# Performance work log

Hardware: AMD Instinct MI355X
Metric: run time of the kernel (lower is better)

Reference implementation:

```python
import jax, jax.numpy as jnp
import numpy as np

N = 50000   # nodes
E = 400000  # directed edges (line-graph nodes)
LE = 1600000  # line-graph edges
B = 256     # graphs in batch
F = 64      # n_feats
ED = 16     # edge_dim
NIT = 3     # n_iter
SF = 6 * F  # LinearBlock hidden


def _seg_softmax(vals, seg, num):
    # numerically stable segment softmax (PyG softmax)
    m = jax.ops.segment_max(vals, seg, num_segments=num)
    e = jnp.exp(vals - m[seg])
    s = jax.ops.segment_sum(e, seg, num_segments=num)
    return e / (s[seg] + 1e-16)


def _gat_pool(out, lg_src, lg_dst, batch, gat_W, att_src, att_dst, gat_bias):
    # PyG GATConv(F, 1): heads=1, add_self_loops=True, negative_slope=0.2
    xw = out @ gat_W                       # [E, 1]
    sl = jnp.arange(E, dtype=lg_src.dtype)
    src = jnp.concatenate([lg_src, sl])
    dst = jnp.concatenate([lg_dst, sl])
    a_s = xw[:, 0] * att_src[0]
    a_d = xw[:, 0] * att_dst[0]
    alpha = jax.nn.leaky_relu(a_s[src] + a_d[dst], negative_slope=0.2)
    coef = _seg_softmax(alpha, dst, E)     # softmax over incoming line-edges
    xc = jax.ops.segment_sum(coef[:, None] * xw[src], dst, num_segments=E) + gat_bias  # [E,1]
    # GlobalAttentionPool: segment softmax over batch, then weighted sum pool
    sc = _seg_softmax(xc[:, 0], batch, B)[:, None]
    return jax.ops.segment_sum(out * sc, batch, num_segments=B)  # [B, F]


def _bn(x, g, b):
    # BatchNorm1d in training mode (batch stats, biased var, eps=1e-5)
    m = x.mean(0)
    v = ((x - m) ** 2).mean(0)
    return (x - m) * jax.lax.rsqrt(v + 1e-5) * g + b


def _prelu(x, w):
    return jnp.where(x >= 0, x, w * x)


def _lin_block(x, bn1_g, bn1_b, W1, b1, bn_g, bn_b, pr, W, b, bn5_g, bn5_b, pr5, W5, b5):
    x = _bn(x, bn1_g, bn1_b) @ W1 + b1                       # lin1: [N, 6F]
    h = _prelu(_bn(x, bn_g[0], bn_b[0]), pr[0]) @ W[0] + b[0]  # lin2
    h = _prelu(_bn(h, bn_g[1], bn_b[1]), pr[1]) @ W[1] + b[1]  # lin3
    x = (h + x) / 2
    x = (_prelu(_bn(x, bn_g[2], bn_b[2]), pr[2]) @ W[2] + b[2] + x) / 2  # lin4
    x = _prelu(_bn(x, bn5_g, bn5_b), pr5) @ W5 + b5          # lin5: [N, F]
    return x


def setup_inputs() -> dict:
    key = jax.random.key(0)
    ks = jax.random.split(key, 20)
    def nrm(k, shape, s=0.1):
        return jax.random.normal(k, shape, jnp.float32) * s
    inp = {}
    inp["x"] = jax.random.normal(ks[0], (N, F), jnp.float32)
    inp["edge_attr"] = jax.random.normal(ks[1], (E, ED), jnp.float32)
    inp["edge_index"] = jax.random.randint(ks[2], (2, E), 0, N, jnp.int32)
    inp["line_graph_edge_index"] = jax.random.randint(ks[3], (2, LE), 0, E, jnp.int32)
    inp["edge_index_batch"] = jnp.sort(jax.random.randint(ks[4], (E,), 0, B, jnp.int32))
    inp["W_u"] = nrm(ks[5], (F, F)); inp["W_v"] = nrm(ks[6], (F, F)); inp["W_e"] = nrm(ks[7], (ED, F))
    inp["gat_W"] = nrm(ks[8], (F, 1)); inp["gat_att_src"] = nrm(ks[9], (1,)); inp["gat_att_dst"] = nrm(ks[10], (1,))
    inp["gat_bias"] = jnp.zeros((1,), jnp.float32)
    inp["a"] = nrm(ks[11], (1, F, NIT)); inp["a_bias"] = jnp.zeros((1, 1, NIT), jnp.float32)
    inp["W_gout"] = nrm(ks[12], (F, F)); inp["b_gout"] = jnp.zeros((F,), jnp.float32)
    inp["lb_bn1_g"] = jnp.ones((F,), jnp.float32); inp["lb_bn1_b"] = jnp.zeros((F,), jnp.float32)
    inp["lb_W1"] = nrm(ks[13], (F, SF)); inp["lb_b1"] = jnp.zeros((SF,), jnp.float32)
    inp["lb_bn_g"] = jnp.ones((3, SF), jnp.float32); inp["lb_bn_b"] = jnp.zeros((3, SF), jnp.float32)
    inp["lb_pr"] = jnp.full((3,), 0.25, jnp.float32)
    inp["lb_W"] = nrm(ks[14], (3, SF, SF)); inp["lb_b"] = jnp.zeros((3, SF), jnp.float32)
    inp["lb_bn5_g"] = jnp.ones((SF,), jnp.float32); inp["lb_bn5_b"] = jnp.zeros((SF,), jnp.float32)
    inp["lb_pr5"] = jnp.array(0.25, jnp.float32)
    inp["lb_W5"] = nrm(ks[15], (SF, F)); inp["lb_b5"] = jnp.zeros((F,), jnp.float32)
    return inp


def reference(x, edge_attr, W_u, W_v, W_e, gat_W, gat_att_src, gat_att_dst, gat_bias,
              a, a_bias, W_gout, b_gout,
              lb_bn1_g, lb_bn1_b, lb_W1, lb_b1, lb_bn_g, lb_bn_b, lb_pr, lb_W, lb_b,
              lb_bn5_g, lb_bn5_b, lb_pr5, lb_W5, lb_b5,
              edge_index, line_graph_edge_index, edge_index_batch):
    ei0, ei1 = edge_index[0], edge_index[1]
    lg0, lg1 = line_graph_edge_index[0], line_graph_edge_index[1]
    # initial directed-edge features
    ea = ((x @ W_u)[ei0] + (x @ W_v)[ei1] + edge_attr @ W_e) / 3.0  # [E, F]
    out = ea
    outs, gouts = [], []
    for _ in range(NIT):
        out = ea + jax.ops.segment_sum(out[lg0], lg1, num_segments=E)  # line-graph message passing
        gout = _gat_pool(out, lg0, lg1, edge_index_batch, gat_W, gat_att_src, gat_att_dst, gat_bias)
        outs.append(out)
        gouts.append(jnp.tanh(gout @ W_gout + b_gout))
    out_all = jnp.stack(outs, -1)    # [E, F, NIT]
    gout_all = jnp.stack(gouts, -1)  # [B, F, NIT]
    sc = jax.nn.softmax((gout_all * a).sum(1, keepdims=True) + a_bias, axis=-1)  # [B,1,NIT]
    out = (out_all * sc[edge_index_batch]).sum(-1)  # per-edge gather == repeat_interleave(degree)
    xn = x + jax.ops.segment_sum(out, ei1, num_segments=N)
    return _lin_block(xn, lb_bn1_g, lb_bn1_b, lb_W1, lb_b1, lb_bn_g, lb_bn_b, lb_pr, lb_W, lb_b,
                      lb_bn5_g, lb_bn5_b, lb_pr5, lb_W5, lb_b5)
```

## Files before the change

### kernel.cpp

```cpp
#include <hip/hip_runtime.h>
#include <math.h>

#define NN 50000
#define EE 400000
#define LEE 1600000
#define BBATCH 256
#define FF 64
#define EDD 16
#define NITER 3
#define SFD 384

#define CDIV(a,b) (((a)+(b)-1)/(b))

typedef unsigned short ushort_t;
typedef __attribute__((ext_vector_type(8))) short bf16x8;
typedef __attribute__((ext_vector_type(4))) float f32x4;

__device__ inline float b2f(ushort_t u) { return __uint_as_float(((unsigned)u) << 16); }
__device__ inline ushort_t f2b(float f) {
    unsigned u = __float_as_uint(f);
    return (ushort_t)((u + 0x7fffu + ((u >> 16) & 1u)) >> 16);
}

__global__ void k_hist(const int* __restrict__ idx, int n, int* __restrict__ cnt) {
    int i = blockIdx.x * blockDim.x + threadIdx.x;
    if (i < n) atomicAdd(&cnt[idx[i]], 1);
}
__global__ void k_part(const int* __restrict__ in, int n, int* __restrict__ part) {
    __shared__ int s[256];
    int i = blockIdx.x * 256 + threadIdx.x;
    s[threadIdx.x] = (i < n) ? in[i] : 0;
    __syncthreads();
    for (int off = 128; off > 0; off >>= 1) {
        if (threadIdx.x < off) s[threadIdx.x] += s[threadIdx.x + off];
        __syncthreads();
    }
    if (threadIdx.x == 0) part[blockIdx.x] = s[0];
}
__global__ void k_scan_single(int* __restrict__ a, int n) {
    __shared__ int s[256];
    int v = (threadIdx.x < n) ? a[threadIdx.x] : 0;
    s[threadIdx.x] = v; __syncthreads();
    for (int off = 1; off < 256; off <<= 1) {
        int t = (threadIdx.x >= off) ? s[threadIdx.x - off] : 0;
        __syncthreads(); s[threadIdx.x] += t; __syncthreads();
    }
    if (threadIdx.x < n) a[threadIdx.x] = s[threadIdx.x] - v;
}
__global__ void k_scan_add(int* __restrict__ a, int n, const int* __restrict__ off) {
    __shared__ int s[256];
    int i = blockIdx.x * 256 + threadIdx.x;
    int v = (i < n) ? a[i] : 0;
    s[threadIdx.x] = v; __syncthreads();
    for (int o = 1; o < 256; o <<= 1) {
        int t = (threadIdx.x >= o) ? s[threadIdx.x - o] : 0;
        __syncthreads(); s[threadIdx.x] += t; __syncthreads();
    }
    if (i < n) a[i] = s[threadIdx.x] - v + off[blockIdx.x];
}
__global__ void k_scan_out(const int* __restrict__ in, int n, const int* __restrict__ boff,
                           int* __restrict__ out) {
    __shared__ int s[256];
    int i = blockIdx.x * 256 + threadIdx.x;
    int v = (i < n) ? in[i] : 0;
    s[threadIdx.x] = v; __syncthreads();
    for (int o = 1; o < 256; o <<= 1) {
        int t = (threadIdx.x >= o) ? s[threadIdx.x - o] : 0;
        __syncthreads(); s[threadIdx.x] += t; __syncthreads();
    }
    if (i < n) out[i] = s[threadIdx.x] - v + boff[blockIdx.x];
    if (i == n - 1) out[n] = s[threadIdx.x] + boff[blockIdx.x];
}
__global__ void k_fill_lg(const int* __restrict__ lg, const int* __restrict__ rowptr,
                          int* __restrict__ cnt, int* __restrict__ srcidx) {
    int i = blockIdx.x * blockDim.x + threadIdx.x;
    if (i >= LEE) return;
    int d = lg[LEE + i];
    int pos = rowptr[d] + atomicAdd(&cnt[d], 1);
    srcidx[pos] = lg[i];
}
__global__ void k_fill_n(const int* __restrict__ ei, const int* __restrict__ rowptr,
                         int* __restrict__ cnt, int* __restrict__ nidx) {
    int i = blockIdx.x * blockDim.x + threadIdx.x;
    if (i >= EE) return;
    int d = ei[EE + i];
    int pos = rowptr[d] + atomicAdd(&cnt[d], 1);
    nidx[pos] = i;
}


__global__ void k_node_mm(const float* __restrict__ x, const float* __restrict__ Wu,
                          const float* __restrict__ Wv, float* __restrict__ xu,
                          float* __restrict__ xv) {
    __shared__ float su[64 * 64];
    __shared__ float sv[64 * 64];
    int tid = threadIdx.x;
    for (int i = tid; i < 64 * 64; i += blockDim.x) { su[i] = Wu[i]; sv[i] = Wv[i]; }
    __syncthreads();
    int row = blockIdx.x * 4 + (tid >> 6);
    int f = tid & 63;
    if (row >= NN) return;
    const float* xr = x + (long long)row * 64;
    float au = 0.f, av = 0.f;
    #pragma unroll
    for (int k = 0; k < 64; ++k) {
        float xv_ = xr[k];
        au += xv_ * su[k * 64 + f];
        av += xv_ * sv[k * 64 + f];
    }
    xu[(long long)row * 64 + f] = au;
    xv[(long long)row * 64 + f] = av;
}

__global__ void k_ea_b16(const float* __restrict__ xu, const float* __restrict__ xv,
                         const float* __restrict__ eattr, const float* __restrict__ We,
                         const int* __restrict__ ei, ushort_t* __restrict__ eab) {
    __shared__ float swe[16 * 64];
    int tid = threadIdx.x;
    for (int i = tid; i < 1024; i += 256) swe[i] = We[i];
    __syncthreads();
    int e = blockIdx.x * 4 + (tid >> 6);
    int f = tid & 63;
    if (e >= EE) return;
    int s = ei[e];
    int d = ei[EE + e];
    const float* ar = eattr + (long long)e * 16;
    float acc = 0.f;
    #pragma unroll
    for (int k = 0; k < 16; ++k) acc += ar[k] * swe[k * 64 + f];
    float v = (xu[(long long)s * 64 + f] + xv[(long long)d * 64 + f] + acc) * (1.0f / 3.0f);
    eab[(long long)e * 64 + f] = f2b(v);
}

__global__ void k_mp_gather(const ushort_t* __restrict__ prev,
                            const ushort_t* __restrict__ eab,
                            const int* __restrict__ rowptr, const int* __restrict__ srcidx,
                            const float* __restrict__ gatW,
                            ushort_t* __restrict__ outb, float* __restrict__ xw) {
    int tid = threadIdx.x;
    int d = blockIdx.x * 4 + (tid >> 6);
    int f = tid & 63;
    if (d >= EE) return;
    float acc = b2f(eab[(long long)d * 64 + f]);
    int p0 = rowptr[d], p1 = rowptr[d + 1];
    int j = p0;
    for (; j + 4 <= p1; j += 4) {
        int s0 = srcidx[j], s1 = srcidx[j + 1], s2 = srcidx[j + 2], s3 = srcidx[j + 3];
        float v0 = b2f(prev[(long long)s0 * 64 + f]);
        float v1 = b2f(prev[(long long)s1 * 64 + f]);
        float v2 = b2f(prev[(long long)s2 * 64 + f]);
        float v3 = b2f(prev[(long long)s3 * 64 + f]);
        acc += (v0 + v1) + (v2 + v3);
    }
    for (; j < p1; ++j)
        acc += b2f(prev[(long long)srcidx[j] * 64 + f]);
    outb[(long long)d * 64 + f] = f2b(acc);
    float w = acc * gatW[f];
    #pragma unroll
    for (int o = 32; o > 0; o >>= 1) w += __shfl_down(w, o, 64);
    if (f == 0) xw[d] = w;
}

__global__ void k_gat_fused(const float* __restrict__ xw,
                            const int* __restrict__ rowptr, const int* __restrict__ srcidx,
                            const float* __restrict__ att_s, const float* __restrict__ att_d,
                            const float* __restrict__ gbias, float* __restrict__ xc) {
    int e = blockIdx.x * blockDim.x + threadIdx.x;
    if (e >= EE) return;
    float as = att_s[0], ad = att_d[0];
    float xwd = xw[e];
    float adt = xwd * ad;
    float aself = xwd * as + adt;
    if (aself < 0.f) aself *= 0.2f;
    int p0 = rowptr[e], p1 = rowptr[e + 1];
    float m = aself;
    for (int j = p0; j < p1; ++j) {
        float a = xw[srcidx[j]] * as + adt;
        if (a < 0.f) a *= 0.2f;
        m = fmaxf(m, a);
    }
    float ssum = expf(aself - m);
    float wsum = ssum * xwd;
    for (int j = p0; j < p1; ++j) {
        float xs = xw[srcidx[j]];
        float a = xs * as + adt;
        if (a < 0.f) a *= 0.2f;
        float ev = expf(a - m);
        ssum += ev;
        wsum += ev * xs;
    }
    xc[e] = wsum / (ssum + 1e-16f) + gbias[0];
}

__global__ void k_batchptr(const int* __restrict__ batch, int* __restrict__ bptr) {
    int e = blockIdx.x * blockDim.x + threadIdx.x;
    if (e >= EE) return;
    int b = batch[e];
    int bp = (e == 0) ? -1 : batch[e - 1];
    for (int q = bp + 1; q <= b; ++q) bptr[q] = e;
    if (e == EE - 1)
        for (int q = b + 1; q <= BBATCH; ++q) bptr[q] = EE;
}

__global__ void k_pool(const float* __restrict__ xc, const ushort_t* __restrict__ out,
                       const int* __restrict__ bptr, float* __restrict__ gout) {
    int b = blockIdx.x;
    int p0 = bptr[b], p1 = bptr[b + 1];
    __shared__ float red[256];
    int tid = threadIdx.x;
    float mx = -INFINITY;
    for (int e = p0 + tid; e < p1; e += 256) mx = fmaxf(mx, xc[e]);
    red[tid] = mx; __syncthreads();
    for (int s = 128; s > 0; s >>= 1) { if (tid < s) red[tid] = fmaxf(red[tid], red[tid + s]); __syncthreads(); }
    float m = red[0]; __syncthreads();
    float sm = 0.f;
    for (int e = p0 + tid; e < p1; e += 256) sm += expf(xc[e] - m);
    red[tid] = sm; __syncthreads();
    for (int s = 128; s > 0; s >>= 1) { if (tid < s) red[tid] += red[tid + s]; __syncthreads(); }
    float ssum = red[0] + 1e-16f; __syncthreads();
    int f = tid & 63, chunk = tid >> 6;
    float acc = 0.f;
    for (int e = p0 + chunk; e < p1; e += 4) {
        float w = expf(xc[e] - m);
        acc += w * b2f(out[(long long)e * 64 + f]);
    }
    red[tid] = acc; __syncthreads();
    if (chunk == 0) {
        float tot = red[f] + red[64 + f] + red[128 + f] + red[192 + f];
        gout[b * 64 + f] = tot / ssum;
    }
}

__global__ void k_gout_mm(const float* __restrict__ gout, const float* __restrict__ Wg,
                          const float* __restrict__ bg, float* __restrict__ gt) {
    __shared__ float sw[64 * 64];
    int tid = threadIdx.x;
    for (int i = tid; i < 4096; i += blockDim.x) sw[i] = Wg[i];
    __syncthreads();
    int row = blockIdx.x * 4 + (tid >> 6);
    int f = tid & 63;
    if (row >= BBATCH) return;
    const float* gr = gout + row * 64;
    float acc = bg[f];
    #pragma unroll
    for (int k = 0; k < 64; ++k) acc += gr[k] * sw[k * 64 + f];
    gt[row * 64 + f] = tanhf(acc);
}

__global__ void k_att(const float* __restrict__ g0, const float* __restrict__ g1,
                      const float* __restrict__ g2, const float* __restrict__ a,
                      const float* __restrict__ abias, float* __restrict__ sc) {
    int b = blockIdx.x;
    int f = threadIdx.x;
    float v0 = g0[b * 64 + f] * a[f * 3 + 0];
    float v1 = g1[b * 64 + f] * a[f * 3 + 1];
    float v2 = g2[b * 64 + f] * a[f * 3 + 2];
    #pragma unroll
    for (int o = 32; o > 0; o >>= 1) {
        v0 += __shfl_down(v0, o, 64);
        v1 += __shfl_down(v1, o, 64);
        v2 += __shfl_down(v2, o, 64);
    }
    if (f == 0) {
        float s0 = v0 + abias[0], s1 = v1 + abias[1], s2 = v2 + abias[2];
        float m = fmaxf(s0, fmaxf(s1, s2));
        float e0 = expf(s0 - m), e1 = expf(s1 - m), e2 = expf(s2 - m);
        float inv = 1.0f / (e0 + e1 + e2);
        sc[b * 3 + 0] = e0 * inv; sc[b * 3 + 1] = e1 * inv; sc[b * 3 + 2] = e2 * inv;
    }
}

__global__ void k_comb(ushort_t* __restrict__ o1, const ushort_t* __restrict__ o2,
                       const ushort_t* __restrict__ o3, const float* __restrict__ sc,
                       const int* __restrict__ batch) {
    long long idx = (long long)blockIdx.x * blockDim.x + threadIdx.x;
    if (idx >= (long long)EE * 64) return;
    int e = (int)(idx >> 6);
    int b = batch[e];
    float v = b2f(o1[idx]) * sc[b * 3] + b2f(o2[idx]) * sc[b * 3 + 1] + b2f(o3[idx]) * sc[b * 3 + 2];
    o1[idx] = f2b(v);
}

__global__ void k_node_gather(const ushort_t* __restrict__ comb, const int* __restrict__ nrow,
                              const int* __restrict__ nidx, const float* __restrict__ x,
                              float* __restrict__ xn) {
    int tid = threadIdx.x;
    int n = blockIdx.x * 4 + (tid >> 6);
    int f = tid & 63;
    if (n >= NN) return;
    float acc = x[(long long)n * 64 + f];
    int p0 = nrow[n], p1 = nrow[n + 1];
    int j = p0;
    for (; j + 4 <= p1; j += 4) {
        int e0 = nidx[j], e1 = nidx[j + 1], e2 = nidx[j + 2], e3 = nidx[j + 3];
        float v0 = b2f(comb[(long long)e0 * 64 + f]);
        float v1 = b2f(comb[(long long)e1 * 64 + f]);
        float v2 = b2f(comb[(long long)e2 * 64 + f]);
        float v3 = b2f(comb[(long long)e3 * 64 + f]);
        acc += (v0 + v1) + (v2 + v3);
    }
    for (; j < p1; ++j) acc += b2f(comb[(long long)nidx[j] * 64 + f]);
    xn[(long long)n * 64 + f] = acc;
}

__global__ void k_colstats(const float* __restrict__ X, int ncols, int nrows,
                           float* __restrict__ csum, float* __restrict__ csumsq) {
    int c = threadIdx.x;
    int rpb = CDIV(nrows, (int)gridDim.x);
    int r0 = blockIdx.x * rpb;
    int r1 = min(r0 + rpb, nrows);
    float s = 0.f, s2 = 0.f;
    for (int r = r0; r < r1; ++r) {
        float v = X[(long long)r * ncols + c];
        s += v; s2 += v * v;
    }
    atomicAdd(&csum[c], s);
    atomicAdd(&csumsq[c], s2);
}

__global__ void k_bnfin(const float* __restrict__ csum, const float* __restrict__ csumsq,
                        int ncols, float* __restrict__ meanv, float* __restrict__ invv) {
    int c = blockIdx.x * blockDim.x + threadIdx.x;
    if (c >= ncols) return;
    float m = csum[c] * (1.0f / NN);
    float var = csumsq[c] * (1.0f / NN) - m * m;
    meanv[c] = m;
    invv[c] = rsqrtf(var + 1e-5f);
}

__global__ __launch_bounds__(256) void k_gemm_bn_mfma(
    const float* __restrict__ A, const float* __restrict__ W,
    const float* __restrict__ bias, const float* __restrict__ res,
    const float* __restrict__ meanv, const float* __restrict__ invv,
    const float* __restrict__ g, const float* __restrict__ bb,
    const float* __restrict__ pr, float scale,
    int nrows, int K, int M, float* __restrict__ C) {
    __shared__ ushort_t sA[64][40];
    __shared__ ushort_t sB[64][40];
    __shared__ float sScl[SFD], sOff[SFD];
    int tid = threadIdx.x;
    int wave = tid >> 6, lane = tid & 63;
    int l16 = lane & 15, klo = lane >> 4;
    long long rowBase = (long long)blockIdx.y * 64;
    int colBase = blockIdx.x * 64;
    int wr = (wave >> 1) * 32, wc = (wave & 1) * 32;
    float prs = pr ? pr[0] : 1.0f;
    for (int c = tid; c < K; c += 256) {
        float scl = invv[c] * g[c];
        sScl[c] = scl;
        sOff[c] = bb[c] - meanv[c] * scl;
    }
    __syncthreads();
    f32x4 acc[2][2] = {};
    for (int k0 = 0; k0 < K; k0 += 32) {
        #pragma unroll
        for (int rep = 0; rep < 2; ++rep) {
            int i4 = (rep * 256 + tid) * 4;
            int r = i4 >> 5, kk = i4 & 31;
            long long gr = rowBase + r;
            float fv[4] = {0.f, 0.f, 0.f, 0.f};
            if (gr < nrows) {
                const float4 v = *(const float4*)&A[gr * K + k0 + kk];
                fv[0] = v.x; fv[1] = v.y; fv[2] = v.z; fv[3] = v.w;
            }
            union { ushort_t u[4]; uint2 v2; } pk;
            #pragma unroll
            for (int j = 0; j < 4; ++j) {
                int c = k0 + kk + j;
                float t = fv[j] * sScl[c] + sOff[c];
                if (t < 0.f) t *= prs;
                pk.u[j] = f2b(t);
            }
            *(uint2*)&sA[r][kk] = pk.v2;
        }
        {
            int col = lane;
            int kbase = wave * 8;
            union { ushort_t u[8]; uint4 v4; } pk;
            #pragma unroll
            for (int i = 0; i < 8; ++i)
                pk.u[i] = f2b(W[(long long)(k0 + kbase + i) * M + colBase + col]);
            *(uint4*)&sB[col][kbase] = pk.v4;
        }
        __syncthreads();
        bf16x8 af[2], bf[2];
        #pragma unroll
        for (int m = 0; m < 2; ++m)
            af[m] = *(const bf16x8*)&sA[wr + m * 16 + l16][klo * 8];
        #pragma unroll
        for (int n = 0; n < 2; ++n)
            bf[n] = *(const bf16x8*)&sB[wc + n * 16 + l16][klo * 8];
        #pragma unroll
        for (int m = 0; m < 2; ++m)
            #pragma unroll
            for (int n = 0; n < 2; ++n)
                acc[m][n] = __builtin_amdgcn_mfma_f32_16x16x32_bf16(af[m], bf[n], acc[m][n], 0, 0, 0);
        __syncthreads();
    }
    #pragma unroll
    for (int m = 0; m < 2; ++m) {
        #pragma unroll
        for (int n = 0; n < 2; ++n) {
            int col = colBase + wc + n * 16 + l16;
            long long row0 = rowBase + wr + m * 16 + klo * 4;
            #pragma unroll
            for (int r = 0; r < 4; ++r) {
                long long row = row0 + r;
                if (row < nrows) {
                    float v = acc[m][n][r] + bias[col];
                    if (res) v += res[row * M + col];
                    C[row * M + col] = v * scale;
                }
            }
        }
    }
}

extern "C" void kernel_launch(void* const* d_in, const int* in_sizes, int n_in,
                              void* d_out, int out_size, void* d_ws, size_t ws_size,
                              hipStream_t stream) {
    const float* x       = (const float*)d_in[0];
    const float* eattr   = (const float*)d_in[1];
    const int*   ei      = (const int*)d_in[2];
    const int*   lg      = (const int*)d_in[3];
    const int*   batch   = (const int*)d_in[4];
    const float* W_u     = (const float*)d_in[5];
    const float* W_v     = (const float*)d_in[6];
    const float* W_e     = (const float*)d_in[7];
    const float* gat_W   = (const float*)d_in[8];
    const float* att_s   = (const float*)d_in[9];
    const float* att_d   = (const float*)d_in[10];
    const float* gat_b   = (const float*)d_in[11];
    const float* a_att   = (const float*)d_in[12];
    const float* a_bias  = (const float*)d_in[13];
    const float* W_gout  = (const float*)d_in[14];
    const float* b_gout  = (const float*)d_in[15];
    const float* bn1_g   = (const float*)d_in[16];
    const float* bn1_b   = (const float*)d_in[17];
    const float* lb_W1   = (const float*)d_in[18];
    const float* lb_b1   = (const float*)d_in[19];
    const float* lb_bn_g = (const float*)d_in[20];
    const float* lb_bn_b = (const float*)d_in[21];
    const float* lb_pr   = (const float*)d_in[22];
    const float* lb_W    = (const float*)d_in[23];
    const float* lb_b    = (const float*)d_in[24];
    const float* bn5_g   = (const float*)d_in[25];
    const float* bn5_b   = (const float*)d_in[26];
    const float* pr5     = (const float*)d_in[27];
    const float* lb_W5   = (const float*)d_in[28];
    const float* lb_b5   = (const float*)d_in[29];
    float* out_final = (float*)d_out;

    const long long ESZ = (long long)EE * FF;
    const long long NSZ = (long long)NN * FF;
    char* cur = (char*)d_ws;
    auto alloc = [&](size_t bytes) -> void* {
        void* p = (void*)cur;
        cur += (bytes + 255) & ~(size_t)255;
        return p;
    };
    float* XU = (float*)alloc(NSZ * 4);
    float* XV = (float*)alloc(NSZ * 4);
    ushort_t* O1 = (ushort_t*)alloc(ESZ * 2);
    ushort_t* O2 = (ushort_t*)alloc(ESZ * 2);
    ushort_t* O3 = (ushort_t*)alloc(ESZ * 2);
    float* XW = (float*)alloc((size_t)EE * 4);
    float* XC = (float*)alloc((size_t)EE * 4);
    float* XN = (float*)alloc(NSZ * 4);
    float* GRAW = (float*)alloc(BBATCH * FF * 4);
    float* G0 = (float*)alloc(BBATCH * FF * 4);
    float* G1 = (float*)alloc(BBATCH * FF * 4);
    float* G2 = (float*)alloc(BBATCH * FF * 4);
    float* SCATT = (float*)alloc(BBATCH * 3 * 4);
    int* BPTR = (int*)alloc((BBATCH + 1) * 4);
    int* LROW = (int*)alloc((size_t)(EE + 1) * 4);
    int* LSRC = (int*)alloc((size_t)LEE * 4);
    int* LCNT = (int*)alloc((size_t)EE * 4);
    int* NROW = (int*)alloc((size_t)(NN + 1) * 4);
    int* NIDX = (int*)alloc((size_t)EE * 4);
    int* NCNT = (int*)alloc((size_t)NN * 4);
    int* SP0 = (int*)alloc(2048 * 4);
    int* SP1 = (int*)alloc(256 * 4);
    float* CSUM = (float*)alloc(SFD * 4);
    float* CSUMSQ = (float*)alloc(SFD * 4);
    float* MEANV = (float*)alloc(SFD * 4);
    float* INVV = (float*)alloc(SFD * 4);
    if ((size_t)(cur - (char*)d_ws) > ws_size) return;

    float* T1 = (float*)O1;
    float* T2 = T1 + (long long)NN * SFD;
    float* GTS[3] = {G0, G1, G2};

    k_node_mm<<<CDIV(NN, 4), 256, 0, stream>>>(x, W_u, W_v, XU, XV);
    k_batchptr<<<CDIV(EE, 256), 256, 0, stream>>>(batch, BPTR);

    {
        hipMemsetAsync(LCNT, 0, (size_t)EE * 4, stream);
        k_hist<<<CDIV(LEE, 256), 256, 0, stream>>>(lg + LEE, LEE, LCNT);
        int nb0 = CDIV(EE, 256), nb1 = CDIV(nb0, 256);
        k_part<<<nb0, 256, 0, stream>>>(LCNT, EE, SP0);
        k_part<<<nb1, 256, 0, stream>>>(SP0, nb0, SP1);
        k_scan_single<<<1, 256, 0, stream>>>(SP1, nb1);
        k_scan_add<<<nb1, 256, 0, stream>>>(SP0, nb0, SP1);
        k_scan_out<<<nb0, 256, 0, stream>>>(LCNT, EE, SP0, LROW);
        hipMemsetAsync(LCNT, 0, (size_t)EE * 4, stream);
        k_fill_lg<<<CDIV(LEE, 256), 256, 0, stream>>>(lg, LROW, LCNT, LSRC);
    }
    {
        hipMemsetAsync(NCNT, 0, (size_t)NN * 4, stream);
        k_hist<<<CDIV(EE, 256), 256, 0, stream>>>(ei + EE, EE, NCNT);
        int nb0 = CDIV(NN, 256), nb1 = CDIV(nb0, 256);
        k_part<<<nb0, 256, 0, stream>>>(NCNT, NN, SP0);
        k_part<<<nb1, 256, 0, stream>>>(SP0, nb0, SP1);
        k_scan_single<<<1, 256, 0, stream>>>(SP1, nb1);
        k_scan_add<<<nb1, 256, 0, stream>>>(SP0, nb0, SP1);
        k_scan_out<<<nb0, 256, 0, stream>>>(NCNT, NN, SP0, NROW);
        hipMemsetAsync(NCNT, 0, (size_t)NN * 4, stream);
        k_fill_n<<<CDIV(EE, 256), 256, 0, stream>>>(ei, NROW, NCNT, NIDX);
    }

    const int EB = CDIV(EE, 4);

    auto gat_pool = [&](ushort_t* buf, int t) {
        k_gat_fused<<<CDIV(EE, 256), 256, 0, stream>>>(XW, LROW, LSRC, att_s, att_d, gat_b, XC);
        k_pool<<<BBATCH, 256, 0, stream>>>(XC, buf, BPTR, GRAW);
        k_gout_mm<<<CDIV(BBATCH, 4), 256, 0, stream>>>(GRAW, W_gout, b_gout, GTS[t]);
    };

    k_ea_b16<<<EB, 256, 0, stream>>>(XU, XV, eattr, W_e, ei, O3);
    k_mp_gather<<<EB, 256, 0, stream>>>(O3, O3, LROW, LSRC, gat_W, O1, XW);
    gat_pool(O1, 0);
    k_mp_gather<<<EB, 256, 0, stream>>>(O1, O3, LROW, LSRC, gat_W, O2, XW);
    gat_pool(O2, 1);
    k_mp_gather<<<EB, 256, 0, stream>>>(O2, O3, LROW, LSRC, gat_W, O3, XW);
    gat_pool(O3, 2);

    k_att<<<BBATCH, 64, 0, stream>>>(G0, G1, G2, a_att, a_bias, SCATT);
    k_comb<<<(int)CDIV(ESZ, 256), 256, 0, stream>>>(O1, O2, O3, SCATT, batch);
    k_node_gather<<<CDIV(NN, 4), 256, 0, stream>>>(O1, NROW, NIDX, x, XN);

    hipMemsetAsync(CSUM, 0, 2 * SFD * 4, stream);
    k_colstats<<<256, FF, 0, stream>>>(XN, FF, NN, CSUM, CSUMSQ);
    k_bnfin<<<CDIV(FF, 64), 64, 0, stream>>>(CSUM, CSUMSQ, FF, MEANV, INVV);
    {
        dim3 g(SFD / 64, CDIV(NN, 64));
        k_gemm_bn_mfma<<<g, 256, 0, stream>>>(XN, lb_W1, lb_b1, nullptr, MEANV, INVV,
                                              bn1_g, bn1_b, nullptr, 1.0f, NN, FF, SFD, T1);
    }
    hipMemsetAsync(CSUM, 0, 2 * SFD * 4, stream);
    k_colstats<<<256, SFD, 0, stream>>>(T1, SFD, NN, CSUM, CSUMSQ);
    k_bnfin<<<CDIV(SFD, 64), 64, 0, stream>>>(CSUM, CSUMSQ, SFD, MEANV, INVV);
    {
        dim3 g(SFD / 64, CDIV(NN, 64));
        k_gemm_bn_mfma<<<g, 256, 0, stream>>>(T1, lb_W, lb_b, nullptr, MEANV, INVV,
                                              lb_bn_g, lb_bn_b, lb_pr, 1.0f, NN, SFD, SFD, T2);
    }
    hipMemsetAsync(CSUM, 0, 2 * SFD * 4, stream);
    k_colstats<<<256, SFD, 0, stream>>>(T2, SFD, NN, CSUM, CSUMSQ);
    k_bnfin<<<CDIV(SFD, 64), 64, 0, stream>>>(CSUM, CSUMSQ, SFD, MEANV, INVV);
    {
        dim3 g(SFD / 64, CDIV(NN, 64));
        k_gemm_bn_mfma<<<g, 256, 0, stream>>>(T2, lb_W + (long long)SFD * SFD, lb_b + SFD, T1,
                                              MEANV, INVV, lb_bn_g + SFD, lb_bn_b + SFD,
                                              lb_pr + 1, 0.5f, NN, SFD, SFD, T1);
    }
    hipMemsetAsync(CSUM, 0, 2 * SFD * 4, stream);
    k_colstats<<<256, SFD, 0, stream>>>(T1, SFD, NN, CSUM, CSUMSQ);
    k_bnfin<<<CDIV(SFD, 64), 64, 0, stream>>>(CSUM, CSUMSQ, SFD, MEANV, INVV);
    {
        dim3 g(SFD / 64, CDIV(NN, 64));
        k_gemm_bn_mfma<<<g, 256, 0, stream>>>(T1, lb_W + 2LL * SFD * SFD, lb_b + 2 * SFD, T1,
                                              MEANV, INVV, lb_bn_g + 2 * SFD, lb_bn_b + 2 * SFD,
                                              lb_pr + 2, 0.5f, NN, SFD, SFD, T2);
    }
    hipMemsetAsync(CSUM, 0, 2 * SFD * 4, stream);
    k_colstats<<<256, SFD, 0, stream>>>(T2, SFD, NN, CSUM, CSUMSQ);
    k_bnfin<<<CDIV(SFD, 64), 64, 0, stream>>>(CSUM, CSUMSQ, SFD, MEANV, INVV);
    {
        dim3 g(FF / 64, CDIV(NN, 64));
        k_gemm_bn_mfma<<<g, 256, 0, stream>>>(T2, lb_W5, lb_b5, nullptr, MEANV, INVV,
                                              bn5_g, bn5_b, pr5, 1.0f, NN, SFD, FF, out_final);
    }
}
```

Measured before the change: 2.136 ms.

## Store intermediates in bf16, fuse BN stats into GEMM epilogues, vectorize gathers

The LinearBlock intermediates, the node features and the node matmul outputs are now stored as bf16 instead of fp32. Column sum and sum-of-squares for batch norm are accumulated with atomics in each GEMM epilogue, which removes the separate colstats and bnfin kernels. Each GEMM block now covers a 64-row stripe across all output columns and computes mean and variance from the raw sums itself. The edge gather kernels process two bf16 features per lane to halve the number of load instructions. The cost is lower precision in stored activations, more atomics, and redundant loading of the full W into LDS for every row block.

Result: slower. 2.204 ms (+3.2%).

```diff
diff --git a/kernel.cpp b/kernel.cpp
--- a/kernel.cpp
+++ b/kernel.cpp
@@ -90,8 +90,8 @@
 
 
 __global__ void k_node_mm(const float* __restrict__ x, const float* __restrict__ Wu,
-                          const float* __restrict__ Wv, float* __restrict__ xu,
-                          float* __restrict__ xv) {
+                          const float* __restrict__ Wv, ushort_t* __restrict__ xu,
+                          ushort_t* __restrict__ xv) {
     __shared__ float su[64 * 64];
     __shared__ float sv[64 * 64];
     int tid = threadIdx.x;
@@ -108,28 +108,35 @@
         au += xv_ * su[k * 64 + f];
         av += xv_ * sv[k * 64 + f];
     }
-    xu[(long long)row * 64 + f] = au;
-    xv[(long long)row * 64 + f] = av;
-}
-
-__global__ void k_ea_b16(const float* __restrict__ xu, const float* __restrict__ xv,
+    xu[(long long)row * 64 + f] = f2b(au);
+    xv[(long long)row * 64 + f] = f2b(av);
+}
+
+__global__ void k_ea_b16(const ushort_t* __restrict__ xu, const ushort_t* __restrict__ xv,
                          const float* __restrict__ eattr, const float* __restrict__ We,
                          const int* __restrict__ ei, ushort_t* __restrict__ eab) {
     __shared__ float swe[16 * 64];
     int tid = threadIdx.x;
     for (int i = tid; i < 1024; i += 256) swe[i] = We[i];
     __syncthreads();
-    int e = blockIdx.x * 4 + (tid >> 6);
-    int f = tid & 63;
+    int e = blockIdx.x * 8 + (tid >> 5);
+    int f2 = (tid & 31) * 2;
     if (e >= EE) return;
     int s = ei[e];
     int d = ei[EE + e];
+    unsigned us = *(const unsigned*)&xu[(long long)s * 64 + f2];
+    unsigned ud = *(const unsigned*)&xv[(long long)d * 64 + f2];
     const float* ar = eattr + (long long)e * 16;
-    float acc = 0.f;
+    float a0 = 0.f, a1 = 0.f;
     #pragma unroll
-    for (int k = 0; k < 16; ++k) acc += ar[k] * swe[k * 64 + f];
-    float v = (xu[(long long)s * 64 + f] + xv[(long long)d * 64 + f] + acc) * (1.0f / 3.0f);
-    eab[(long long)e * 64 + f] = f2b(v);
+    for (int k = 0; k < 16; ++k) {
+        float w = ar[k];
+        a0 += w * swe[k * 64 + f2];
+        a1 += w * swe[k * 64 + f2 + 1];
+    }
+    float v0 = (b2f((ushort_t)us) + b2f((ushort_t)ud) + a0) * (1.0f / 3.0f);
+    float v1 = (b2f((ushort_t)(us >> 16)) + b2f((ushort_t)(ud >> 16)) + a1) * (1.0f / 3.0f);
+    *(unsigned*)&eab[(long long)e * 64 + f2] = (unsigned)f2b(v0) | ((unsigned)f2b(v1) << 16);
 }
 
 __global__ void k_mp_gather(const ushort_t* __restrict__ prev,
@@ -138,27 +145,33 @@
                             const float* __restrict__ gatW,
                             ushort_t* __restrict__ outb, float* __restrict__ xw) {
     int tid = threadIdx.x;
-    int d = blockIdx.x * 4 + (tid >> 6);
-    int f = tid & 63;
+    int d = blockIdx.x * 8 + (tid >> 5);
+    int f2 = (tid & 31) * 2;
     if (d >= EE) return;
-    float acc = b2f(eab[(long long)d * 64 + f]);
+    unsigned ue = *(const unsigned*)&eab[(long long)d * 64 + f2];
+    float a0 = b2f((ushort_t)ue), a1 = b2f((ushort_t)(ue >> 16));
     int p0 = rowptr[d], p1 = rowptr[d + 1];
     int j = p0;
     for (; j + 4 <= p1; j += 4) {
         int s0 = srcidx[j], s1 = srcidx[j + 1], s2 = srcidx[j + 2], s3 = srcidx[j + 3];
-        float v0 = b2f(prev[(long long)s0 * 64 + f]);
-        float v1 = b2f(prev[(long long)s1 * 64 + f]);
-        float v2 = b2f(prev[(long long)s2 * 64 + f]);
-        float v3 = b2f(prev[(long long)s3 * 64 + f]);
-        acc += (v0 + v1) + (v2 + v3);
-    }
-    for (; j < p1; ++j)
-        acc += b2f(prev[(long long)srcidx[j] * 64 + f]);
-    outb[(long long)d * 64 + f] = f2b(acc);
-    float w = acc * gatW[f];
+        unsigned u0 = *(const unsigned*)&prev[(long long)s0 * 64 + f2];
+        unsigned u1 = *(const unsigned*)&prev[(long long)s1 * 64 + f2];
+        unsigned u2 = *(const unsigned*)&prev[(long long)s2 * 64 + f2];
+        unsigned u3 = *(const unsigned*)&prev[(long long)s3 * 64 + f2];
+        a0 += (b2f((ushort_t)u0) + b2f((ushort_t)u1)) + (b2f((ushort_t)u2) + b2f((ushort_t)u3));
+        a1 += (b2f((ushort_t)(u0 >> 16)) + b2f((ushort_t)(u1 >> 16))) +
+              (b2f((ushort_t)(u2 >> 16)) + b2f((ushort_t)(u3 >> 16)));
+    }
+    for (; j < p1; ++j) {
+        unsigned u0 = *(const unsigned*)&prev[(long long)srcidx[j] * 64 + f2];
+        a0 += b2f((ushort_t)u0);
+        a1 += b2f((ushort_t)(u0 >> 16));
+    }
+    *(unsigned*)&outb[(long long)d * 64 + f2] = (unsigned)f2b(a0) | ((unsigned)f2b(a1) << 16);
+    float w = a0 * gatW[f2] + a1 * gatW[f2 + 1];
     #pragma unroll
-    for (int o = 32; o > 0; o >>= 1) w += __shfl_down(w, o, 64);
-    if (f == 0) xw[d] = w;
+    for (int o = 16; o > 0; o >>= 1) w += __shfl_down(w, o, 32);
+    if ((tid & 31) == 0) xw[d] = w;
 }
 
 __global__ void k_gat_fused(const float* __restrict__ xw,
@@ -283,7 +296,7 @@
 
 __global__ void k_node_gather(const ushort_t* __restrict__ comb, const int* __restrict__ nrow,
                               const int* __restrict__ nidx, const float* __restrict__ x,
-                              float* __restrict__ xn) {
+                              ushort_t* __restrict__ xnb) {
     int tid = threadIdx.x;
     int n = blockIdx.x * 4 + (tid >> 6);
     int f = tid & 63;
@@ -300,117 +313,116 @@
         acc += (v0 + v1) + (v2 + v3);
     }
     for (; j < p1; ++j) acc += b2f(comb[(long long)nidx[j] * 64 + f]);
-    xn[(long long)n * 64 + f] = acc;
-}
-
-__global__ void k_colstats(const float* __restrict__ X, int ncols, int nrows,
-                           float* __restrict__ csum, float* __restrict__ csumsq) {
+    xnb[(long long)n * 64 + f] = f2b(acc);
+}
+
+__global__ void k_colstats_b16(const ushort_t* __restrict__ X, int ncols, int nrows,
+                               float* __restrict__ csum, float* __restrict__ csumsq) {
     int c = threadIdx.x;
     int rpb = CDIV(nrows, (int)gridDim.x);
     int r0 = blockIdx.x * rpb;
     int r1 = min(r0 + rpb, nrows);
     float s = 0.f, s2 = 0.f;
     for (int r = r0; r < r1; ++r) {
-        float v = X[(long long)r * ncols + c];
+        float v = b2f(X[(long long)r * ncols + c]);
         s += v; s2 += v * v;
     }
     atomicAdd(&csum[c], s);
     atomicAdd(&csumsq[c], s2);
 }
 
-__global__ void k_bnfin(const float* __restrict__ csum, const float* __restrict__ csumsq,
-                        int ncols, float* __restrict__ meanv, float* __restrict__ invv) {
-    int c = blockIdx.x * blockDim.x + threadIdx.x;
-    if (c >= ncols) return;
-    float m = csum[c] * (1.0f / NN);
-    float var = csumsq[c] * (1.0f / NN) - m * m;
-    meanv[c] = m;
-    invv[c] = rsqrtf(var + 1e-5f);
-}
-
-__global__ __launch_bounds__(256) void k_gemm_bn_mfma(
-    const float* __restrict__ A, const float* __restrict__ W,
-    const float* __restrict__ bias, const float* __restrict__ res,
-    const float* __restrict__ meanv, const float* __restrict__ invv,
+template<int MT>
+__global__ __launch_bounds__(512) void k_gemm_lb(
+    const ushort_t* __restrict__ A, const float* __restrict__ W,
+    const float* __restrict__ bias, const ushort_t* __restrict__ resb,
+    const float* __restrict__ csum, const float* __restrict__ csumsq,
     const float* __restrict__ g, const float* __restrict__ bb,
-    const float* __restrict__ pr, float scale,
-    int nrows, int K, int M, float* __restrict__ C) {
+    const float* __restrict__ pr, float scale, int nrows, int K,
+    ushort_t* __restrict__ Cb, float* __restrict__ Cf,
+    float* __restrict__ osum, float* __restrict__ osumsq) {
+    constexpr int NF = MT / 32;
     __shared__ ushort_t sA[64][40];
-    __shared__ ushort_t sB[64][40];
+    __shared__ ushort_t sB[MT][40];
     __shared__ float sScl[SFD], sOff[SFD];
     int tid = threadIdx.x;
     int wave = tid >> 6, lane = tid & 63;
     int l16 = lane & 15, klo = lane >> 4;
-    long long rowBase = (long long)blockIdx.y * 64;
-    int colBase = blockIdx.x * 64;
-    int wr = (wave >> 1) * 32, wc = (wave & 1) * 32;
+    int rowg = wave >> 1, colg = wave & 1;
+    long long rowBase = (long long)blockIdx.x * 64;
     float prs = pr ? pr[0] : 1.0f;
-    for (int c = tid; c < K; c += 256) {
-        float scl = invv[c] * g[c];
+    const float invn = 1.0f / (float)NN;
+    for (int c = tid; c < K; c += 512) {
+        float mean = csum[c] * invn;
+        float var = csumsq[c] * invn - mean * mean;
+        float scl = rsqrtf(var + 1e-5f) * g[c];
         sScl[c] = scl;
-        sOff[c] = bb[c] - meanv[c] * scl;
+        sOff[c] = bb[c] - mean * scl;
     }
     __syncthreads();
-    f32x4 acc[2][2] = {};
+    f32x4 acc[NF] = {};
     for (int k0 = 0; k0 < K; k0 += 32) {
-        #pragma unroll
-        for (int rep = 0; rep < 2; ++rep) {
-            int i4 = (rep * 256 + tid) * 4;
+        {
+            int i4 = tid * 4;
             int r = i4 >> 5, kk = i4 & 31;
             long long gr = rowBase + r;
-            float fv[4] = {0.f, 0.f, 0.f, 0.f};
+            unsigned lo = 0, hi = 0;
             if (gr < nrows) {
-                const float4 v = *(const float4*)&A[gr * K + k0 + kk];
-                fv[0] = v.x; fv[1] = v.y; fv[2] = v.z; fv[3] = v.w;
+                const ushort_t* ap = &A[gr * K + k0 + kk];
+                unsigned raw0 = *(const unsigned*)ap;
+                unsigned raw1 = *(const unsigned*)(ap + 2);
+                float t0 = b2f((ushort_t)raw0) * sScl[k0 + kk] + sOff[k0 + kk];
+                float t1 = b2f((ushort_t)(raw0 >> 16)) * sScl[k0 + kk + 1] + sOff[k0 + kk + 1];
+                float t2 = b2f((ushort_t)raw1) * sScl[k0 + kk + 2] + sOff[k0 + kk + 2];
+                float t3 = b2f((ushort_t)(raw1 >> 16)) * sScl[k0 + kk + 3] + sOff[k0 + kk + 3];
+                if (t0 < 0.f) t0 *= prs;
+                if (t1 < 0.f) t1 *= prs;
+                if (t2 < 0.f) t2 *= prs;
+                if (t3 < 0.f) t3 *= prs;
+                lo = (unsigned)f2b(t0) | ((unsigned)f2b(t1) << 16);
+                hi = (unsigned)f2b(t2) | ((unsigned)f2b(t3) << 16);
             }
-            union { ushort_t u[4]; uint2 v2; } pk;
-            #pragma unroll
-            for (int j = 0; j < 4; ++j) {
-                int c = k0 + kk + j;
-                float t = fv[j] * sScl[c] + sOff[c];
-                if (t < 0.f) t *= prs;
-                pk.u[j] = f2b(t);
-            }
-            *(uint2*)&sA[r][kk] = pk.v2;
+            uint2 pk; pk.x = lo; pk.y = hi;
+            *(uint2*)&sA[r][kk] = pk;
         }
-        {
-            int col = lane;
-            int kbase = wave * 8;
-            union { ushort_t u[8]; uint4 v4; } pk;
-            #pragma unroll
-            for (int i = 0; i < 8; ++i)
-                pk.u[i] = f2b(W[(long long)(k0 + kbase + i) * M + colBase + col]);
-            *(uint4*)&sB[col][kbase] = pk.v4;
+        for (int i = tid; i < 32 * MT; i += 512) {
+            int col = i % MT, kk = i / MT;
+            sB[col][kk] = f2b(W[(long long)(k0 + kk) * MT + col]);
         }
         __syncthreads();
-        bf16x8 af[2], bf[2];
+        bf16x8 af = *(const bf16x8*)&sA[rowg * 16 + l16][klo * 8];
         #pragma unroll
-        for (int m = 0; m < 2; ++m)
-            af[m] = *(const bf16x8*)&sA[wr + m * 16 + l16][klo * 8];
+        for (int n = 0; n < NF; ++n) {
+            bf16x8 bf = *(const bf16x8*)&sB[colg * (MT / 2) + n * 16 + l16][klo * 8];
+            acc[n] = __builtin_amdgcn_mfma_f32_16x16x32_bf16(af, bf, acc[n], 0, 0, 0);
+        }
+        __syncthreads();
+    }
+    #pragma unroll
+    for (int n = 0; n < NF; ++n) {
+        int col = colg * (MT / 2) + n * 16 + l16;
+        long long row0 = rowBase + rowg * 16 + klo * 4;
+        float bcol = bias[col];
+        float s = 0.f, s2 = 0.f;
         #pragma unroll
-        for (int n = 0; n < 2; ++n)
-            bf[n] = *(const bf16x8*)&sB[wc + n * 16 + l16][klo * 8];
-        #pragma unroll
-        for (int m = 0; m < 2; ++m)
-            #pragma unroll
-            for (int n = 0; n < 2; ++n)
-                acc[m][n] = __builtin_amdgcn_mfma_f32_16x16x32_bf16(af[m], bf[n], acc[m][n], 0, 0, 0);
-        __syncthreads();
-    }
-    #pragma unroll
-    for (int m = 0; m < 2; ++m) {
-        #pragma unroll
-        for (int n = 0; n < 2; ++n) {
-            int col = colBase + wc + n * 16 + l16;
-            long long row0 = rowBase + wr + m * 16 + klo * 4;
-            #pragma unroll
-            for (int r = 0; r < 4; ++r) {
-                long long row = row0 + r;
-                if (row < nrows) {
-                    float v = acc[m][n][r] + bias[col];
-                    if (res) v += res[row * M + col];
-                    C[row * M + col] = v * scale;
-                }
+        for (int r = 0; r < 4; ++r) {
+            long long row = row0 + r;
+            if (row < nrows) {
+                float v = acc[n][r] + bcol;
+                if (resb) v += b2f(resb[row * MT + col]);
+                v *= scale;
+                if (Cf) Cf[row * MT + col] = v;
+                if (Cb) Cb[row * MT + col] = f2b(v);
+                s += v; s2 += v * v;
+            }
+        }
+        if (osum) {
+            s += __shfl_down(s, 32, 64);
+            s2 += __shfl_down(s2, 32, 64);
+            s += __shfl_down(s, 16, 64);
+            s2 += __shfl_down(s2, 16, 64);
+            if (lane < 16) {
+                atomicAdd(&osum[col], s);
+                atomicAdd(&osumsq[col], s2);
             }
         }
     }
@@ -459,14 +471,14 @@
         cur += (bytes + 255) & ~(size_t)255;
         return p;
     };
-    float* XU = (float*)alloc(NSZ * 4);
-    float* XV = (float*)alloc(NSZ * 4);
+    ushort_t* XU = (ushort_t*)alloc(NSZ * 2);
+    ushort_t* XV = (ushort_t*)alloc(NSZ * 2);
     ushort_t* O1 = (ushort_t*)alloc(ESZ * 2);
     ushort_t* O2 = (ushort_t*)alloc(ESZ * 2);
     ushort_t* O3 = (ushort_t*)alloc(ESZ * 2);
     float* XW = (float*)alloc((size_t)EE * 4);
     float* XC = (float*)alloc((size_t)EE * 4);
-    float* XN = (float*)alloc(NSZ * 4);
+    ushort_t* XNB = (ushort_t*)alloc(NSZ * 2);
     float* GRAW = (float*)alloc(BBATCH * FF * 4);
     float* G0 = (float*)alloc(BBATCH * FF * 4);
     float* G1 = (float*)alloc(BBATCH * FF * 4);
@@ -481,15 +493,18 @@
     int* NCNT = (int*)alloc((size_t)NN * 4);
     int* SP0 = (int*)alloc(2048 * 4);
     int* SP1 = (int*)alloc(256 * 4);
-    float* CSUM = (float*)alloc(SFD * 4);
-    float* CSUMSQ = (float*)alloc(SFD * 4);
-    float* MEANV = (float*)alloc(SFD * 4);
-    float* INVV = (float*)alloc(SFD * 4);
+    float* STATS = (float*)alloc(5 * 2 * SFD * 4);
     if ((size_t)(cur - (char*)d_ws) > ws_size) return;
 
-    float* T1 = (float*)O1;
-    float* T2 = T1 + (long long)NN * SFD;
+    ushort_t* T1B = O1;
+    ushort_t* T2B = T1B + (long long)NN * SFD;
+    ushort_t* T3B = T2B + (long long)NN * SFD;
+    ushort_t* T4B = T3B + (long long)NN * SFD;
+    float* CS[5][2];
+    for (int i = 0; i < 5; ++i) { CS[i][0] = STATS + i * 2 * SFD; CS[i][1] = CS[i][0] + SFD; }
     float* GTS[3] = {G0, G1, G2};
+
+    hipMemsetAsync(STATS, 0, 5 * 2 * SFD * 4, stream);
 
     k_node_mm<<<CDIV(NN, 4), 256, 0, stream>>>(x, W_u, W_v, XU, XV);
     k_batchptr<<<CDIV(EE, 256), 256, 0, stream>>>(batch, BPTR);
@@ -519,7 +534,7 @@
         k_fill_n<<<CDIV(EE, 256), 256, 0, stream>>>(ei, NROW, NCNT, NIDX);
     }
 
-    const int EB = CDIV(EE, 4);
+    const int EB8 = CDIV(EE, 8);
 
     auto gat_pool = [&](ushort_t* buf, int t) {
         k_gat_fused<<<CDIV(EE, 256), 256, 0, stream>>>(XW, LROW, LSRC, att_s, att_d, gat_b, XC);
@@ -527,58 +542,33 @@
         k_gout_mm<<<CDIV(BBATCH, 4), 256, 0, stream>>>(GRAW, W_gout, b_gout, GTS[t]);
     };
 
-    k_ea_b16<<<EB, 256, 0, stream>>>(XU, XV, eattr, W_e, ei, O3);
-    k_mp_gather<<<EB, 256, 0, stream>>>(O3, O3, LROW, LSRC, gat_W, O1, XW);
+    k_ea_b16<<<EB8, 256, 0, stream>>>(XU, XV, eattr, W_e, ei, O3);
+    k_mp_gather<<<EB8, 256, 0, stream>>>(O3, O3, LROW, LSRC, gat_W, O1, XW);
     gat_pool(O1, 0);
-    k_mp_gather<<<EB, 256, 0, stream>>>(O1, O3, LROW, LSRC, gat_W, O2, XW);
+    k_mp_gather<<<EB8, 256, 0, stream>>>(O1, O3, LROW, LSRC, gat_W, O2, XW);
     gat_pool(O2, 1);
-    k_mp_gather<<<EB, 256, 0, stream>>>(O2, O3, LROW, LSRC, gat_W, O3, XW);
+    k_mp_gather<<<EB8, 256, 0, stream>>>(O2, O3, LROW, LSRC, gat_W, O3, XW);
     gat_pool(O3, 2);
 
     k_att<<<BBATCH, 64, 0, stream>>>(G0, G1, G2, a_att, a_bias, SCATT);
     k_comb<<<(int)CDIV(ESZ, 256), 256, 0, stream>>>(O1, O2, O3, SCATT, batch);
-    k_node_gather<<<CDIV(NN, 4), 256, 0, stream>>>(O1, NROW, NIDX, x, XN);
-
-    hipMemsetAsync(CSUM, 0, 2 * SFD * 4, stream);
-    k_colstats<<<256, FF, 0, stream>>>(XN, FF, NN, CSUM, CSUMSQ);
-    k_bnfin<<<CDIV(FF, 64), 64, 0, stream>>>(CSUM, CSUMSQ, FF, MEANV, INVV);
-    {
-        dim3 g(SFD / 64, CDIV(NN, 64));
-        k_gemm_bn_mfma<<<g, 256, 0, stream>>>(XN, lb_W1, lb_b1, nullptr, MEANV, INVV,
-                                              bn1_g, bn1_b, nullptr, 1.0f, NN, FF, SFD, T1);
-    }
-    hipMemsetAsync(CSUM, 0, 2 * SFD * 4, stream);
-    k_colstats<<<256, SFD, 0, stream>>>(T1, SFD, NN, CSUM, CSUMSQ);
-    k_bnfin<<<CDIV(SFD, 64), 64, 0, stream>>>(CSUM, CSUMSQ, SFD, MEANV, INVV);
-    {
-        dim3 g(SFD / 64, CDIV(NN, 64));
-        k_gemm_bn_mfma<<<g, 256, 0, stream>>>(T1, lb_W, lb_b, nullptr, MEANV, INVV,
-                                              lb_bn_g, lb_bn_b, lb_pr, 1.0f, NN, SFD, SFD, T2);
-    }
-    hipMemsetAsync(CSUM, 0, 2 * SFD * 4, stream);
-    k_colstats<<<256, SFD, 0, stream>>>(T2, SFD, NN, CSUM, CSUMSQ);
-    k_bnfin<<<CDIV(SFD, 64), 64, 0, stream>>>(CSUM, CSUMSQ, SFD, MEANV, INVV);
-    {
-        dim3 g(SFD / 64, CDIV(NN, 64));
-        k_gemm_bn_mfma<<<g, 256, 0, stream>>>(T2, lb_W + (long long)SFD * SFD, lb_b + SFD, T1,
-                                              MEANV, INVV, lb_bn_g + SFD, lb_bn_b + SFD,
-                                              lb_pr + 1, 0.5f, NN, SFD, SFD, T1);
-    }
-    hipMemsetAsync(CSUM, 0, 2 * SFD * 4, stream);
-    k_colstats<<<256, SFD, 0, stream>>>(T1, SFD, NN, CSUM, CSUMSQ);
-    k_bnfin<<<CDIV(SFD, 64), 64, 0, stream>>>(CSUM, CSUMSQ, SFD, MEANV, INVV);
-    {
-        dim3 g(SFD / 64, CDIV(NN, 64));
-        k_gemm_bn_mfma<<<g, 256, 0, stream>>>(T1, lb_W + 2LL * SFD * SFD, lb_b + 2 * SFD, T1,
-                                              MEANV, INVV, lb_bn_g + 2 * SFD, lb_bn_b + 2 * SFD,
-                                              lb_pr + 2, 0.5f, NN, SFD, SFD, T2);
-    }
-    hipMemsetAsync(CSUM, 0, 2 * SFD * 4, stream);
-    k_colstats<<<256, SFD, 0, stream>>>(T2, SFD, NN, CSUM, CSUMSQ);
-    k_bnfin<<<CDIV(SFD, 64), 64, 0, stream>>>(CSUM, CSUMSQ, SFD, MEANV, INVV);
-    {
-        dim3 g(FF / 64, CDIV(NN, 64));
-        k_gemm_bn_mfma<<<g, 256, 0, stream>>>(T2, lb_W5, lb_b5, nullptr, MEANV, INVV,
-                                              bn5_g, bn5_b, pr5, 1.0f, NN, SFD, FF, out_final);
-    }
-}
+    k_node_gather<<<CDIV(NN, 4), 256, 0, stream>>>(O1, NROW, NIDX, x, XNB);
+    k_colstats_b16<<<256, FF, 0, stream>>>(XNB, FF, NN, CS[0][0], CS[0][1]);
+
+    const int GB = CDIV(NN, 64);
+    k_gemm_lb<384><<<GB, 512, 0, stream>>>(XNB, lb_W1, lb_b1, nullptr,
+        CS[0][0], CS[0][1], bn1_g, bn1_b, nullptr, 1.0f, NN, FF,
+        T1B, nullptr, CS[1][0], CS[1][1]);
+    k_gemm_lb<384><<<GB, 512, 0, stream>>>(T1B, lb_W, lb_b, nullptr,
+        CS[1][0], CS[1][1], lb_bn_g, lb_bn_b, lb_pr, 1.0f, NN, SFD,
+        T2B, nullptr, CS[2][0], CS[2][1]);
+    k_gemm_lb<384><<<GB, 512, 0, stream>>>(T2B, lb_W + (long long)SFD * SFD, lb_b + SFD, T1B,
+        CS[2][0], CS[2][1], lb_bn_g + SFD, lb_bn_b + SFD, lb_pr + 1, 0.5f, NN, SFD,
+        T3B, nullptr, CS[3][0], CS[3][1]);
+    k_gemm_lb<384><<<GB, 512, 0, stream>>>(T3B, lb_W + 2LL * SFD * SFD, lb_b + 2 * SFD, T3B,
+        CS[3][0], CS[3][1], lb_bn_g + 2 * SFD, lb_bn_b + 2 * SFD, lb_pr + 2, 0.5f, NN, SFD,
+        T4B, nullptr, CS[4][0], CS[4][1]);
+    k_gemm_lb<64><<<GB, 512, 0, stream>>>(T4B, lb_W5, lb_b5, nullptr,
+        CS[4][0], CS[4][1], bn5_g, bn5_b, pr5, 1.0f, NN, SFD,
+        nullptr, out_final, nullptr, nullptr);
+}
```
